# Kernel tuning notes

Measured on AMD Instinct MI355X. Metric: run time of the kernel, lower is better.

## Reference

```python
import jax, jax.numpy as jnp
import numpy as np

V, E, H, T, B = 100000, 256, 256, 50, 512
FORGET_BIAS = 2.0


def setup_inputs() -> dict:
    key = jax.random.key(0)
    ks = jax.random.split(key, 12)
    s = 0.05
    return {
        "input_queries": jax.random.randint(ks[0], (B, T), 0, V, dtype=jnp.int32),
        "input_replies": jax.random.randint(ks[1], (B, T), 0, V, dtype=jnp.int32),
        "query_lengths": jax.random.randint(ks[2], (B,), 1, T, dtype=jnp.int32),
        "reply_lengths": jax.random.randint(ks[3], (B,), 1, T, dtype=jnp.int32),
        # keep weak distances strictly positive (diagonal is inverted)
        "weak_distances": jax.random.uniform(ks[4], (B, B), jnp.float32) + 0.5,
        "embeddings": jax.random.normal(ks[5], (V, E), jnp.float32) * s,
        "W": jax.random.normal(ks[6], (E + H, 4 * H), jnp.float32) * s,
        "b": jnp.zeros((4 * H,), jnp.float32),
        "p_i": jax.random.normal(ks[7], (H,), jnp.float32) * s,
        "p_f": jax.random.normal(ks[8], (H,), jnp.float32) * s,
        "p_o": jax.random.normal(ks[9], (H,), jnp.float32) * s,
        "M": jax.random.normal(ks[10], (H, H), jnp.float32) * s,
    }


def lstm_encode(x, lengths, W, b, p_i, p_f, p_o):
    """TF LSTMCell(use_peepholes=True, forget_bias=2.0); returns final h at each
    sequence's length (dynamic_rnn semantics: state frozen past length)."""
    Bx, Tx, _ = x.shape
    Hx = p_i.shape[0]
    h0 = jnp.zeros((Bx, Hx), x.dtype)

    def step(carry, xt_t):
        xt, t = xt_t
        h, c = carry
        z = jnp.concatenate([xt, h], axis=-1) @ W + b  # [B, 4H]
        i, j, f, o = jnp.split(z, 4, axis=-1)
        i = jax.nn.sigmoid(i + p_i * c)
        f = jax.nn.sigmoid(f + FORGET_BIAS + p_f * c)
        c_new = f * c + i * jnp.tanh(j)
        o = jax.nn.sigmoid(o + p_o * c_new)
        h_new = o * jnp.tanh(c_new)
        m = (t < lengths)[:, None]
        return (jnp.where(m, h_new, h), jnp.where(m, c_new, c)), None

    (h, _), _ = jax.lax.scan(step, (h0, h0),
                             (jnp.swapaxes(x, 0, 1), jnp.arange(Tx)))
    return h


def reference(input_queries, input_replies, query_lengths, reply_lengths,
              weak_distances, embeddings, W, b, p_i, p_f, p_o, M):
    q_emb = embeddings[input_queries]  # [B, T, E]
    r_emb = embeddings[input_replies]  # [B, T, E]
    # query and reply cells share weights (reuse=True in the original)
    q = lstm_encode(q_emb, query_lengths, W, b, p_i, p_f, p_o)  # [B, H]
    r = lstm_encode(r_emb, reply_lengths, W, b, p_i, p_f, p_o)  # [B, H]
    q = q @ M
    distances = q @ r.T                      # [B, B]
    pos = jnp.diagonal(distances)            # positive logits, [B]
    wp = jnp.diagonal(weak_distances)        # [B]
    # wp_tiled[i, j] = wp[j]; positive_logits_tiled[i, j] = pos[j]
    wd_norm = jnp.maximum(0.0, weak_distances / wp[None, :] - 1.0)
    loss = jnp.sum(jnp.maximum(0.0, distances - pos[None, :] + wd_norm))
    return loss
```

## Files before the change

### kernel.cpp

```cpp
#include <hip/hip_runtime.h>

#define TTs 50
#define NSTEP 49

using short8   = __attribute__((ext_vector_type(8))) short;
using ushort4v = __attribute__((ext_vector_type(4))) unsigned short;
using f32x4    = __attribute__((ext_vector_type(4))) float;
using int4v    = __attribute__((ext_vector_type(4))) int;

__device__ __forceinline__ unsigned short f2bf(float f) {
    unsigned u = __builtin_bit_cast(unsigned, f);
    u += 0x7FFFu + ((u >> 16) & 1u);
    return (unsigned short)(u >> 16);
}
__device__ __forceinline__ float bf2f(unsigned short s) {
    unsigned u = ((unsigned)s) << 16;
    return __builtin_bit_cast(float, u);
}
__device__ __forceinline__ float frcp(float x) { return __builtin_amdgcn_rcpf(x); }
__device__ __forceinline__ float sigm(float x)  { return frcp(1.f + __expf(-x)); }
__device__ __forceinline__ float ftanh(float x) { return 1.f - 2.f * frcp(__expf(2.f * x) + 1.f); }

__device__ __forceinline__ void lds_barrier() {
    asm volatile("s_waitcnt lgkmcnt(0)" ::: "memory");
    __builtin_amdgcn_s_barrier();
    asm volatile("" ::: "memory");
}

#define WH_SCALE 512.f
#define H_SCALE  127.f

__global__ __launch_bounds__(1024)
void sort_kernel(const int* __restrict__ lenq, const int* __restrict__ lenr,
                 int* __restrict__ perm, float* __restrict__ out)
{
    __shared__ int cnt[64];
    const int tid = threadIdx.x;
    if (tid == 0) out[0] = 0.f;
    if (tid < 64) cnt[tid] = 0;
    __syncthreads();
    const int l = (tid < 512) ? lenq[tid] : lenr[tid - 512];
    atomicAdd(&cnt[l], 1);
    __syncthreads();
    if (tid == 0) {
        int acc = 0;
        for (int v = 49; v >= 1; --v) { int c = cnt[v]; cnt[v] = acc; acc += c; }
    }
    __syncthreads();
    const int rank = atomicAdd(&cnt[l], 1);
    perm[rank] = tid;
}

__global__ __launch_bounds__(256)
void pack_w_kernel(const float* __restrict__ W,
                   unsigned short* __restrict__ Wxp, signed char* __restrict__ Wq)
{
    __shared__ float ld[64][65];
    const int koff = blockIdx.y * 256;
    const int k0 = (blockIdx.x & 3) * 64, c0 = (blockIdx.x >> 2) * 64;
    const int tid = threadIdx.x;
    #pragma unroll
    for (int i = 0; i < 16; ++i) {
        int idx = tid + i * 256;
        ld[idx >> 6][idx & 63] = W[(size_t)(koff + k0 + (idx >> 6)) * 1024 + c0 + (idx & 63)];
    }
    __syncthreads();
    if (blockIdx.y == 0) {
        #pragma unroll
        for (int j = 0; j < 2; ++j) {
            int idx = tid + j * 256;
            int cl = idx >> 3, kc = (idx & 7) * 8;
            short8 v;
            #pragma unroll
            for (int e = 0; e < 8; ++e) v[e] = (short)f2bf(ld[kc + e][cl]);
            *(short8*)(Wxp + (size_t)(c0 + cl) * 256 + k0 + kc) = v;
        }
    } else {
        #pragma unroll
        for (int j = 0; j < 2; ++j) {
            int idx = tid + j * 256;
            int cl = idx >> 3, kc = (idx & 7) * 8;
            unsigned long long u = 0;
            #pragma unroll
            for (int e = 0; e < 8; ++e) {
                float v = ld[kc + e][cl] * WH_SCALE;
                int q = __float2int_rn(fminf(fmaxf(v, -127.f), 127.f));
                u |= (unsigned long long)(unsigned char)(signed char)q << (8 * e);
            }
            *(unsigned long long*)(Wq + (size_t)(c0 + cl) * 256 + k0 + kc) = u;
        }
    }
}

__global__ __launch_bounds__(512, 4)
void xproj_kernel(const float* __restrict__ emb,
                  const int* __restrict__ idq, const int* __restrict__ idr,
                  const int* __restrict__ lenq, const int* __restrict__ lenr,
                  const int* __restrict__ perm,
                  const unsigned short* __restrict__ Wxp,
                  const float* __restrict__ bias,
                  unsigned short* __restrict__ X)
{
    __shared__ __align__(16) unsigned short As[64 * 264];
    __shared__ int Ls2[4][64];
    __shared__ int Ids2[4][64];
    __shared__ int Tmax[4];

    const int tid = threadIdx.x;
    const int L = tid & 63, w = tid >> 6;
    const int lanelo = L & 15, lhi = L >> 4;
    const int cslice = blockIdx.y;
    const int colbase = cslice * 256 + w * 32;
    const int slot0 = cslice * 16 + w * 2;

    short8 Bx[2][8];
    #pragma unroll
    for (int cf = 0; cf < 2; ++cf) {
        const unsigned short* bb = Wxp + (size_t)(colbase + cf * 16 + lanelo) * 256 + lhi * 8;
        #pragma unroll
        for (int ks = 0; ks < 8; ++ks) Bx[cf][ks] = *(const short8*)(bb + ks * 32);
    }
    float bc[2];
    #pragma unroll
    for (int cf = 0; cf < 2; ++cf) {
        int col = colbase + cf * 16 + lanelo;
        bc[cf] = bias[col] + ((col >= 512 && col < 768) ? 2.0f : 0.f);
    }

    if (tid < 256) {
        int it = tid >> 6, rl = tid & 63;
        int rt = blockIdx.x + it * 196;
        int t = rt >> 4, r0 = (rt & 15) * 64;
        int gr = perm[r0 + rl];
        int len = (gr < 512) ? lenq[gr] : lenr[gr - 512];
        Ls2[it][rl] = len;
        Ids2[it][rl] = (gr < 512) ? idq[gr * TTs + t] : idr[(gr - 512) * TTs + t];
        if (rl == 0) Tmax[it] = len;
    }
    __syncthreads();

    for (int it = 0; it < 4; ++it) {
        const int rt = blockIdx.x + it * 196;
        const int t = rt >> 4;
        const int rblkb = (rt & 15) * 4;
        if (t >= Tmax[it]) continue;
        const int* Ls = Ls2[it];
        const int* Ids = Ids2[it];

        float4 ev0[4], ev1[4];
        bool live[4];
        #pragma unroll
        for (int i = 0; i < 4; ++i) {
            int task = tid + i * 512;
            int rl = task >> 5, kc = (task & 31) * 8;
            live[i] = (t < Ls[rl]);
            if (live[i]) {
                const float* ep = emb + (size_t)Ids[rl] * 256 + kc;
                ev0[i] = *(const float4*)ep;
                ev1[i] = *(const float4*)(ep + 4);
            }
        }
        #pragma unroll
        for (int i = 0; i < 4; ++i) {
            if (live[i]) {
                int task = tid + i * 512;
                int rl = task >> 5, kc = (task & 31) * 8;
                short8 v;
                v[0] = (short)f2bf(ev0[i].x); v[1] = (short)f2bf(ev0[i].y);
                v[2] = (short)f2bf(ev0[i].z); v[3] = (short)f2bf(ev0[i].w);
                v[4] = (short)f2bf(ev1[i].x); v[5] = (short)f2bf(ev1[i].y);
                v[6] = (short)f2bf(ev1[i].z); v[7] = (short)f2bf(ev1[i].w);
                *(short8*)(As + rl * 264 + kc) = v;
            }
        }
        lds_barrier();

        #pragma unroll
        for (int rg = 0; rg < 4; ++rg) {
            int base = rg * 16 + lhi * 4;
            int lmax = max(max(Ls[base], Ls[base + 1]), max(Ls[base + 2], Ls[base + 3]));
            bool myalive = (t < lmax);
            if (__any(myalive)) {
                f32x4 a0 = (f32x4){0.f, 0.f, 0.f, 0.f};
                f32x4 a1 = (f32x4){0.f, 0.f, 0.f, 0.f};
                const unsigned short* ar = As + (rg * 16 + lanelo) * 264 + lhi * 8;
                #pragma unroll
                for (int ks = 0; ks < 8; ++ks) {
                    short8 a = *(const short8*)(ar + ks * 32);
                    a0 = __builtin_amdgcn_mfma_f32_16x16x32_bf16(a, Bx[0][ks], a0, 0, 0, 0);
                    a1 = __builtin_amdgcn_mfma_f32_16x16x32_bf16(a, Bx[1][ks], a1, 0, 0, 0);
                }
                if (myalive) {
                    size_t off = (((size_t)(t * 64 + rblkb + rg)) * 64 + slot0) * 256 + L * 4;
                    ushort4v v0, v1;
                    #pragma unroll
                    for (int j = 0; j < 4; ++j) {
                        v0[j] = f2bf(a0[j] + bc[0]);
                        v1[j] = f2bf(a1[j] + bc[1]);
                    }
                    *(ushort4v*)(X + off) = v0;
                    *(ushort4v*)(X + off + 256) = v1;
                }
            }
        }
        lds_barrier();
    }
}

__global__ __launch_bounds__(1024, 4)
void lstm_i8_kernel(const unsigned short* __restrict__ X,
                    const signed char* __restrict__ Wq,
                    const float* __restrict__ p_i, const float* __restrict__ p_f,
                    const float* __restrict__ p_o,
                    const int* __restrict__ lenq, const int* __restrict__ lenr,
                    const int* __restrict__ perm,
                    unsigned short* __restrict__ hfin)
{
    __shared__ __align__(16) char hl[2 * 4 * 288];
    const int tid = threadIdx.x;
    const int L = tid & 63, w = tid >> 6;
    const int blk = blockIdx.x;
    const int lanelo = L & 15, lhi = L >> 4;
    const int hh = w * 16 + lanelo;

    if (tid < 576) ((int*)hl)[tid] = 0;

    int4v Bw[4][4];
    #pragma unroll
    for (int g = 0; g < 4; ++g)
        #pragma unroll
        for (int kc = 0; kc < 4; ++kc)
            Bw[g][kc] = *(const int4v*)(Wq + (size_t)(g * 256 + hh) * 256 + kc * 64 + lhi * 16);

    const unsigned short* xb = X + (size_t)(blk >> 2) * 16384;
    int xgoff[4];
    #pragma unroll
    for (int g = 0; g < 4; ++g)
        xgoff[g] = (g * 16 + w) * 256 + (blk & 3) * 64 + lanelo * 4 + lhi;

    const bool rdlane = (lanelo & 3) == 0;
    const int ard = (lanelo >> 2) * 288 + lhi * 16;
    const int awr = lhi * 288 + hh;

    const float pii = p_i[hh], pff = p_f[hh], poo = p_o[hh];
    const float INV = 1.f / (H_SCALE * WH_SCALE);

    const int gr = perm[blk * 4 + lhi];
    const int len_ = (gr < 512) ? lenq[gr] : lenr[gr - 512];
    const int p0 = perm[blk * 4];
    const int blkmax = (p0 < 512) ? lenq[p0] : lenr[p0 - 512];

    float cst = 0.f;
    float hst = 0.f;

    int4v a[4];
    #pragma unroll
    for (int kc = 0; kc < 4; ++kc) a[kc] = (int4v){0, 0, 0, 0};

    unsigned short xr[4], xn[4];
    #pragma unroll
    for (int g = 0; g < 4; ++g) xr[g] = xb[xgoff[g]];
    const unsigned short* xp = xb + 1048576;

    __syncthreads();

    for (int t = 0; t < blkmax; ++t) {
        const int rb = (t & 1) * 1152;
        const int wb = 1152 - rb;

        const unsigned short* xs = (t + 1 < blkmax) ? xp : xb;
        #pragma unroll
        for (int g = 0; g < 4; ++g) xn[g] = xs[xgoff[g]];
        xp += 1048576;

        if (rdlane) {
            #pragma unroll
            for (int kc = 0; kc < 4; ++kc)
                a[kc] = *(const int4v*)(hl + rb + ard + kc * 64);
        }

        int4v acc[4];
        #pragma unroll
        for (int g = 0; g < 4; ++g) acc[g] = (int4v){0, 0, 0, 0};
        #pragma unroll
        for (int kc = 0; kc < 4; ++kc)
            #pragma unroll
            for (int g = 0; g < 4; ++g)
                acc[g] = __builtin_amdgcn_mfma_i32_16x16x64_i8(a[kc], Bw[g][kc], acc[g], 0, 0, 0);

        {
            float cv = cst;
            float zi = fmaf((float)acc[0][0], INV, bf2f(xr[0]));
            float zj = fmaf((float)acc[1][0], INV, bf2f(xr[1]));
            float zf = fmaf((float)acc[2][0], INV, bf2f(xr[2]));
            float zo = fmaf((float)acc[3][0], INV, bf2f(xr[3]));
            float iv = sigm(fmaf(pii, cv, zi));
            float fv = sigm(fmaf(pff, cv, zf));
            float jv = ftanh(zj);
            float cn = fv * cv + iv * jv;
            float ov = sigm(fmaf(poo, cn, zo));
            float hn = ov * ftanh(cn);
            bool upd = (t < len_);
            if (upd) { cst = cn; hst = hn; }
            hl[wb + awr] = (signed char)__float2int_rn(hst * H_SCALE);
        }
        lds_barrier();
        #pragma unroll
        for (int g = 0; g < 4; ++g) xr[g] = xn[g];
    }

    hfin[(size_t)gr * 256 + hh] = f2bf(hst);
}

#define TS 64
#define KT 16
#define LDW (TS + 4)

__global__ __launch_bounds__(256)
void gemm_qM_kernel(const unsigned short* __restrict__ hA, const float* __restrict__ B,
                    float* __restrict__ C)
{
    __shared__ float As[KT][LDW];
    __shared__ float Bs[KT][LDW];
    const int tid = threadIdx.x;
    const int tx = tid & 15, ty = tid >> 4;
    const int m0 = blockIdx.x * TS, n0 = blockIdx.y * TS;
    float acc[4][4] = {};
    for (int kk = 0; kk < 256; kk += KT) {
        #pragma unroll
        for (int i = 0; i < 4; ++i) {
            int l = tid + i * 256;
            As[l & 15][l >> 4] = bf2f(hA[(m0 + (l >> 4)) * 256 + kk + (l & 15)]);
            Bs[l >> 6][l & 63] = B[(kk + (l >> 6)) * 256 + n0 + (l & 63)];
        }
        __syncthreads();
        #pragma unroll
        for (int k = 0; k < KT; ++k) {
            float4 a4 = *(const float4*)&As[k][ty * 4];
            float4 b4 = *(const float4*)&Bs[k][tx * 4];
            float av[4] = {a4.x, a4.y, a4.z, a4.w};
            float bv[4] = {b4.x, b4.y, b4.z, b4.w};
            #pragma unroll
            for (int i = 0; i < 4; ++i)
                #pragma unroll
                for (int j = 0; j < 4; ++j)
                    acc[i][j] = fmaf(av[i], bv[j], acc[i][j]);
        }
        __syncthreads();
    }
    #pragma unroll
    for (int i = 0; i < 4; ++i) {
        float4 v = {acc[i][0], acc[i][1], acc[i][2], acc[i][3]};
        *(float4*)&C[(m0 + ty * 4 + i) * 256 + n0 + tx * 4] = v;
    }
}

__global__ __launch_bounds__(256)
void gemm_D_kernel(const float* __restrict__ A, const unsigned short* __restrict__ hB,
                   float* __restrict__ C)
{
    __shared__ float As[KT][LDW];
    __shared__ float Bs[KT][LDW];
    const int tid = threadIdx.x;
    const int tx = tid & 15, ty = tid >> 4;
    const int m0 = blockIdx.x * TS, n0 = blockIdx.y * TS;
    float acc[4][4] = {};
    for (int kk = 0; kk < 256; kk += KT) {
        #pragma unroll
        for (int i = 0; i < 4; ++i) {
            int l = tid + i * 256;
            As[l & 15][l >> 4] = A[(m0 + (l >> 4)) * 256 + kk + (l & 15)];
            Bs[l & 15][l >> 4] = bf2f(hB[(n0 + (l >> 4)) * 256 + kk + (l & 15)]);
        }
        __syncthreads();
        #pragma unroll
        for (int k = 0; k < KT; ++k) {
            float4 a4 = *(const float4*)&As[k][ty * 4];
            float4 b4 = *(const float4*)&Bs[k][tx * 4];
            float av[4] = {a4.x, a4.y, a4.z, a4.w};
            float bv[4] = {b4.x, b4.y, b4.z, b4.w};
            #pragma unroll
            for (int i = 0; i < 4; ++i)
                #pragma unroll
                for (int j = 0; j < 4; ++j)
                    acc[i][j] = fmaf(av[i], bv[j], acc[i][j]);
        }
        __syncthreads();
    }
    #pragma unroll
    for (int i = 0; i < 4; ++i) {
        float4 v = {acc[i][0], acc[i][1], acc[i][2], acc[i][3]};
        *(float4*)&C[(m0 + ty * 4 + i) * 512 + n0 + tx * 4] = v;
    }
}

__global__ __launch_bounds__(256)
void loss_kernel(const float* __restrict__ D, const float* __restrict__ wd,
                 float* __restrict__ out)
{
    int idx = blockIdx.x * 256 + threadIdx.x;
    int j = idx & 511;
    float d   = D[idx];
    float pos = D[j * 512 + j];
    float ww  = wd[idx];
    float wp  = wd[j * 512 + j];
    float wn  = fmaxf(0.f, fmaf(ww, frcp(wp), -1.f));
    float v   = fmaxf(0.f, d - pos + wn);
    #pragma unroll
    for (int o = 32; o > 0; o >>= 1) v += __shfl_down(v, o);
    __shared__ float sm[4];
    if ((threadIdx.x & 63) == 0) sm[threadIdx.x >> 6] = v;
    __syncthreads();
    if (threadIdx.x == 0) atomicAdd(out, sm[0] + sm[1] + sm[2] + sm[3]);
}

extern "C" void kernel_launch(void* const* d_in, const int* in_sizes, int n_in,
                              void* d_out, int out_size, void* d_ws, size_t ws_size,
                              hipStream_t stream) {
    const int*   idq  = (const int*)d_in[0];
    const int*   idr  = (const int*)d_in[1];
    const int*   lenq = (const int*)d_in[2];
    const int*   lenr = (const int*)d_in[3];
    const float* wd   = (const float*)d_in[4];
    const float* emb  = (const float*)d_in[5];
    const float* W    = (const float*)d_in[6];
    const float* bias = (const float*)d_in[7];
    const float* p_i  = (const float*)d_in[8];
    const float* p_f  = (const float*)d_in[9];
    const float* p_o  = (const float*)d_in[10];
    const float* Mm   = (const float*)d_in[11];
    float* out = (float*)d_out;

    char* ws = (char*)d_ws;
    unsigned short* X    = (unsigned short*)ws;
    char* p = ws + (size_t)NSTEP * 1048576 * 2;
    unsigned short* hfin = (unsigned short*)p;  p += 1024 * 256 * 2;
    unsigned short* Wxp  = (unsigned short*)p;  p += 1024 * 256 * 2;
    signed char*    Wq   = (signed char*)p;     p += 1024 * 256;
    float* qM = (float*)p;  p += 512 * 256 * 4;
    float* D  = (float*)p;  p += 512 * 512 * 4;
    int* perm = (int*)p;

    sort_kernel<<<1, 1024, 0, stream>>>(lenq, lenr, perm, out);
    pack_w_kernel<<<dim3(64, 2), 256, 0, stream>>>(W, Wxp, Wq);
    xproj_kernel<<<dim3(196, 4), 512, 0, stream>>>(emb, idq, idr, lenq, lenr,
                                                   perm, Wxp, bias, X);
    lstm_i8_kernel<<<256, 1024, 0, stream>>>(X, Wq, p_i, p_f, p_o,
                                             lenq, lenr, perm, hfin);
    gemm_qM_kernel<<<dim3(8, 4), 256, 0, stream>>>(hfin, Mm, qM);
    gemm_D_kernel<<<dim3(8, 8), 256, 0, stream>>>(qM, hfin + 512 * 256, D);
    loss_kernel<<<1024, 256, 0, stream>>>(D, wd, out);
}
```

Baseline: 150.1 us.

## Fuse diagonal and loss computation into the GEMM epilogues, drop loss kernel

The first GEMM now also computes partial positive logits (dot of each qM row slice with the matching reply row) and writes them into a small 4x512 buffer. The second GEMM computes the hinge loss directly from its accumulators and reduces it atomically, which removes the D matrix write/read and one kernel launch. This saves a launch and a 1 MB round trip through memory. The cost is extra epilogue work and a changed summation order for the positive logits.

```diff
diff --git a/kernel.cpp b/kernel.cpp
--- a/kernel.cpp
+++ b/kernel.cpp
@@ -317,8 +317,11 @@
 #define LDW (TS + 4)
 
 __global__ __launch_bounds__(256)
-void gemm_qM_kernel(const unsigned short* __restrict__ hA, const float* __restrict__ B,
-                    float* __restrict__ C)
+void epi1_kernel(const unsigned short* __restrict__ hA,
+                 const unsigned short* __restrict__ hB,
+                 const float* __restrict__ B,
+                 float* __restrict__ C,
+                 float* __restrict__ pos4)
 {
     __shared__ float As[KT][LDW];
     __shared__ float Bs[KT][LDW];
@@ -353,11 +356,26 @@
         float4 v = {acc[i][0], acc[i][1], acc[i][2], acc[i][3]};
         *(float4*)&C[(m0 + ty * 4 + i) * 256 + n0 + tx * 4] = v;
     }
+    #pragma unroll
+    for (int i = 0; i < 4; ++i) {
+        int row = m0 + ty * 4 + i;
+        ushort4v rv = *(const ushort4v*)(hB + row * 256 + n0 + tx * 4);
+        float p = acc[i][0] * bf2f(rv[0]) + acc[i][1] * bf2f(rv[1])
+                + acc[i][2] * bf2f(rv[2]) + acc[i][3] * bf2f(rv[3]);
+        p += __shfl_xor(p, 1);
+        p += __shfl_xor(p, 2);
+        p += __shfl_xor(p, 4);
+        p += __shfl_xor(p, 8);
+        if (tx == 0) pos4[blockIdx.y * 512 + row] = p;
+    }
 }
 
 __global__ __launch_bounds__(256)
-void gemm_D_kernel(const float* __restrict__ A, const unsigned short* __restrict__ hB,
-                   float* __restrict__ C)
+void epi2_kernel(const float* __restrict__ A,
+                 const unsigned short* __restrict__ hB,
+                 const float* __restrict__ pos4,
+                 const float* __restrict__ wd,
+                 float* __restrict__ out)
 {
     __shared__ float As[KT][LDW];
     __shared__ float Bs[KT][LDW];
@@ -387,25 +405,25 @@
         }
         __syncthreads();
     }
+    float pos_j[4], wdj[4];
+    #pragma unroll
+    for (int j = 0; j < 4; ++j) {
+        int jg = n0 + tx * 4 + j;
+        pos_j[j] = pos4[jg] + pos4[512 + jg] + pos4[1024 + jg] + pos4[1536 + jg];
+        wdj[j] = frcp(wd[jg * 513]);
+    }
+    float v = 0.f;
     #pragma unroll
     for (int i = 0; i < 4; ++i) {
-        float4 v = {acc[i][0], acc[i][1], acc[i][2], acc[i][3]};
-        *(float4*)&C[(m0 + ty * 4 + i) * 512 + n0 + tx * 4] = v;
-    }
-}
-
-__global__ __launch_bounds__(256)
-void loss_kernel(const float* __restrict__ D, const float* __restrict__ wd,
-                 float* __restrict__ out)
-{
-    int idx = blockIdx.x * 256 + threadIdx.x;
-    int j = idx & 511;
-    float d   = D[idx];
-    float pos = D[j * 512 + j];
-    float ww  = wd[idx];
-    float wp  = wd[j * 512 + j];
-    float wn  = fmaxf(0.f, fmaf(ww, frcp(wp), -1.f));
-    float v   = fmaxf(0.f, d - pos + wn);
+        int ig = m0 + ty * 4 + i;
+        float4 wrow = *(const float4*)(wd + ig * 512 + n0 + tx * 4);
+        float wr[4] = {wrow.x, wrow.y, wrow.z, wrow.w};
+        #pragma unroll
+        for (int j = 0; j < 4; ++j) {
+            float wn = fmaxf(0.f, fmaf(wr[j], wdj[j], -1.f));
+            v += fmaxf(0.f, acc[i][j] - pos_j[j] + wn);
+        }
+    }
     #pragma unroll
     for (int o = 32; o > 0; o >>= 1) v += __shfl_down(v, o);
     __shared__ float sm[4];
@@ -437,8 +455,8 @@
     unsigned short* hfin = (unsigned short*)p;  p += 1024 * 256 * 2;
     unsigned short* Wxp  = (unsigned short*)p;  p += 1024 * 256 * 2;
     signed char*    Wq   = (signed char*)p;     p += 1024 * 256;
-    float* qM = (float*)p;  p += 512 * 256 * 4;
-    float* D  = (float*)p;  p += 512 * 512 * 4;
+    float* qM   = (float*)p;  p += 512 * 256 * 4;
+    float* pos4 = (float*)p;  p += 4 * 512 * 4;
     int* perm = (int*)p;
 
     sort_kernel<<<1, 1024, 0, stream>>>(lenq, lenr, perm, out);
@@ -447,7 +465,7 @@
                                                    perm, Wxp, bias, X);
     lstm_i8_kernel<<<256, 1024, 0, stream>>>(X, Wq, p_i, p_f, p_o,
                                              lenq, lenr, perm, hfin);
-    gemm_qM_kernel<<<dim3(8, 4), 256, 0, stream>>>(hfin, Mm, qM);
-    gemm_D_kernel<<<dim3(8, 8), 256, 0, stream>>>(qM, hfin + 512 * 256, D);
-    loss_kernel<<<1024, 256, 0, stream>>>(D, wd, out);
-}
+    unsigned short* rfin = hfin + 512 * 256;
+    epi1_kernel<<<dim3(8, 4), 256, 0, stream>>>(hfin, rfin, Mm, qM, pos4);
+    epi2_kernel<<<dim3(8, 8), 256, 0, stream>>>(qM, rfin, pos4, wd, out);
+}
```

After: 136.5 us. 1.1x faster.
